# Kernel tuning notes

Hardware: AMD Instinct MI355X
Metric: run time of the kernel (lower is better)

Reference implementation:

```python
import jax, jax.numpy as jnp
import numpy as np

D = 2  # NUM_DIM (spatial dimension)


def _mlp(x, params, activate_final=False):
    n = len(params)
    for i, (w, b) in enumerate(params):
        x = x @ w + b
        if i < n - 1 or activate_final:
            x = jnp.tanh(x)
    return x


def _glorot(key, shape):
    fan_in, fan_out = shape[0], shape[-1]
    lim = np.sqrt(6.0 / (fan_in + fan_out)).astype(np.float32)
    return jax.random.uniform(key, shape, jnp.float32, -lim, lim)


def setup_inputs() -> dict:
    key = jax.random.key(0)
    ks = iter(jax.random.split(key, 40))
    B, N, M, K, P, C = 4, 32, 64, 16, 128, 2
    AW, TW, W = 64, 256, 128
    inp = {}
    inp['phase_coords'] = jax.random.normal(next(ks), (B, N, 2 * D), jnp.float32)
    inp['boundary_coords'] = jax.random.normal(next(ks), (B, M, 2 * D), jnp.float32)
    inp['boundary'] = jax.random.uniform(next(ks), (B, M), jnp.float32)
    inp['boundary_weights'] = jax.random.uniform(next(ks), (B, M), jnp.float32)
    inp['position_coords'] = jax.random.normal(next(ks), (B, P, D), jnp.float32)
    inp['sigma'] = jax.random.uniform(next(ks), (B, P, C), jnp.float32)
    inp['velocity_coords'] = jax.random.normal(next(ks), (B, K, D), jnp.float32)
    inp['velocity_weights'] = jax.random.uniform(next(ks), (B, K), jnp.float32)
    inp['scattering_kernel'] = jax.random.uniform(next(ks), (B, N, K), jnp.float32)
    inp['self_scattering_kernel'] = jax.random.uniform(next(ks), (B, K, K), jnp.float32)
    # attention MLP: input 2*D + 2 (coords ++ local frame) -> [64, 64, 1]
    inp['aw0'] = _glorot(next(ks), (2 * D + 2, AW)); inp['ab0'] = jnp.zeros((AW,), jnp.float32)
    inp['aw1'] = _glorot(next(ks), (AW, AW)); inp['ab1'] = jnp.zeros((AW,), jnp.float32)
    inp['aw2'] = _glorot(next(ks), (AW, 1)); inp['ab2'] = jnp.zeros((1,), jnp.float32)
    # transport MLP: input 4*D + C -> [256, 256, 128], activate_final=True
    inp['tw0'] = _glorot(next(ks), (4 * D + C, TW)); inp['tb0'] = jnp.zeros((TW,), jnp.float32)
    inp['tw1'] = _glorot(next(ks), (TW, TW)); inp['tb1'] = jnp.zeros((TW,), jnp.float32)
    inp['tw2'] = _glorot(next(ks), (TW, W)); inp['tb2'] = jnp.zeros((W,), jnp.float32)
    # scattering modules: res_block_depth=2 -> one stacked layer + one final layer
    inp['sw0'] = _glorot(next(ks), (W, W))
    inp['sb0'] = jax.random.uniform(next(ks), (W,), jnp.float32, -0.1, 0.1)
    inp['sw1'] = _glorot(next(ks), (W, W))
    inp['sb1'] = jax.random.uniform(next(ks), (W,), jnp.float32, -0.1, 0.1)
    inp['out_w'] = jax.random.uniform(next(ks), (W,), jnp.float32, -0.1, 0.1)
    return inp


def _forward(phase_coords, boundary_coords, boundary, boundary_weights,
             position_coords, sigma, velocity_coords, velocity_weights,
             scattering_kernel, self_scattering_kernel,
             aw0, ab0, aw1, ab1, aw2, ab2,
             tw0, tb0, tw1, tb1, tw2, tb2,
             sw0, sb0, sw1, sb1, out_w):
    B, N, _ = phase_coords.shape
    M = boundary_coords.shape[1]
    K = velocity_coords.shape[1]
    P = position_coords.shape[1]
    C = sigma.shape[-1]
    K1 = K + 1  # phase velocity v plus the Nv quadrature velocities

    x, v = phase_coords[..., :D], phase_coords[..., D:]          # (B,N,D)
    xp, vp = boundary_coords[..., :D], boundary_coords[..., D:]  # (B,M,D)

    # all velocities at which the transport MLP is evaluated: (B,N,K1,D)
    vall = jnp.concatenate(
        [v[:, :, None, :],
         jnp.broadcast_to(velocity_coords[:, None, :, :], (B, N, K, D))], axis=2)

    # ---- CoefficientNet (geometry-masked MLP attention over coeff positions) ----
    coords = jnp.concatenate(
        [jnp.broadcast_to(x[:, :, None, :], (B, N, K1, D)), vall], axis=-1)  # (B,N,K1,2D)
    ang_g = vall / jnp.sqrt(jnp.sum(vall ** 2, axis=-1, keepdims=True) + 1e-16)
    rel = x[:, :, None, :] - position_coords[:, None, :, :]                 # (B,N,P,D)
    rel_dist = jnp.sqrt(jnp.sum(rel ** 2, axis=-1) + 1e-16)                 # (B,N,P)
    pos_local = jnp.einsum('bnpd,bnkd->bnkp', rel, ang_g)                   # (B,N,K1,P)
    ang_local = pos_local / (rel_dist[:, :, None, :] + 1e-8)
    frames = jnp.stack([ang_local, pos_local], axis=-1)                     # (B,N,K1,P,2)
    qk = jnp.concatenate(
        [jnp.broadcast_to(coords[:, :, :, None, :], (B, N, K1, P, 2 * D)), frames], axis=-1)
    logits = _mlp(qk, [(aw0, ab0), (aw1, ab1), (aw2, ab2)])[..., 0]         # (B,N,K1,P)
    attn_w = jax.nn.softmax(jnp.where(pos_local > 0, logits, -1e30), axis=-1)
    coeff = jnp.exp(-jnp.einsum('bnkp,bpc->bnkc', attn_w, sigma))           # (B,N,K1,C)

    # ---- TransportModule: MLP + exp over (B,N,M,K1) ----
    t_in = jnp.concatenate([
        jnp.broadcast_to(x[:, :, None, None, :], (B, N, M, K1, D)),
        jnp.broadcast_to(vall[:, :, None, :, :], (B, N, M, K1, D)),
        jnp.broadcast_to(xp[:, None, :, None, :], (B, N, M, K1, D)),
        jnp.broadcast_to(vp[:, None, :, None, :], (B, N, M, K1, D)),
        jnp.broadcast_to(coeff[:, :, None, :, :], (B, N, M, K1, C)),
    ], axis=-1)
    g = jnp.exp(_mlp(t_in, [(tw0, tb0), (tw1, tb1), (tw2, tb2)], activate_final=True))
    act_v = g[:, :, :, 0, :]       # (B,N,M,W)  at the phase velocity
    act_vstar = g[:, :, :, 1:, :]  # (B,N,M,K,W) at the quadrature velocities

    rw_v = (1.0 - scattering_kernel) * velocity_weights[:, None, :]        # (B,N,K)
    rw_vs = (1.0 - self_scattering_kernel) * velocity_weights[:, None, :]  # (B,K,K)

    def scat_v(act, sw, sb):
        res = jnp.einsum('bnk,bnmkw->bnmw', rw_v, act)
        return jnp.tanh(jnp.einsum('iw,bnmw->bnmi', sw, res) + sb)

    def scat_vs(act, sw, sb):
        res = jnp.einsum('bij,bnmjw->bnmiw', rw_vs, act)
        return jnp.tanh(jnp.einsum('iw,bnmkw->bnmki', sw, res) + sb)

    # layer_stack block (res_block_depth - 1 = 1 layer, shared params within the layer)
    new_v = act_v + scat_v(act_vstar, sw0, sb0)
    act_vstar = act_vstar + scat_vs(act_vstar, sw0, sb0)
    act_v = new_v
    # final scattering module (fresh params) updating act_v with res_weights_v
    green = act_v + scat_v(act_vstar, sw1, sb1)

    gdot = jnp.einsum('bnmw,w->bnm', green, out_w)
    # quadrature over boundary points
    return jnp.einsum('bnm,bm->bn', gdot, boundary * boundary_weights)


def reference(phase_coords, boundary_coords, boundary, boundary_weights,
              position_coords, sigma, velocity_coords, velocity_weights,
              scattering_kernel, self_scattering_kernel,
              aw0, ab0, aw1, ab1, aw2, ab2,
              tw0, tb0, tw1, tb1, tw2, tb2,
              sw0, sb0, sw1, sb1, out_w):
    return _forward(phase_coords, boundary_coords, boundary, boundary_weights,
                    position_coords, sigma, velocity_coords, velocity_weights,
                    scattering_kernel, self_scattering_kernel,
                    aw0, ab0, aw1, ab1, aw2, ab2,
                    tw0, tb0, tw1, tb1, tw2, tb2,
                    sw0, sb0, sw1, sb1, out_w)
```

## Files before the change

### kernel.cpp

```cpp
#include <hip/hip_runtime.h>
#include <hip/hip_bf16.h>

#define BB 4
#define NN 32
#define MM 64
#define KK 16
#define KK1 17
#define PP 128
#define CC 2

typedef unsigned short ushort_t;
typedef unsigned int uint32;
typedef __attribute__((ext_vector_type(8))) short bhalf8;
typedef __attribute__((ext_vector_type(4))) float floatx4;

__device__ __forceinline__ float fast_tanh(float x) {
    float e = __expf(2.0f * x);
    return 1.0f - 2.0f / (e + 1.0f);
}
__device__ __forceinline__ ushort_t f2b(float f) {
    uint32 u = __float_as_uint(f);
    return (ushort_t)((u + 0x8000u) >> 16);
}
__device__ __forceinline__ float b2f(ushort_t h) {
    return __uint_as_float(((uint32)h) << 16);
}

__global__ void prep_kernel(const float* __restrict__ tw0, const float* __restrict__ tw1,
                            const float* __restrict__ tw2, const float* __restrict__ sw0,
                            const float* __restrict__ sw1, const float* __restrict__ aw0,
                            const float* __restrict__ aw1, const float* __restrict__ tb0,
                            const float* __restrict__ bcoord,
                            ushort_t* __restrict__ W1t, ushort_t* __restrict__ W2t,
                            ushort_t* __restrict__ S0t, ushort_t* __restrict__ S1t,
                            ushort_t* __restrict__ W0a, ushort_t* __restrict__ W1a,
                            ushort_t* __restrict__ w_ws) {
    int i = blockIdx.x * 256 + threadIdx.x;
    if (i < 65536) {
        int nn = i >> 8, k = i & 255;
        W1t[i] = f2b(tw1[k * 256 + nn]);
    } else if (i < 98304) {
        int j = i - 65536; int nn = j >> 8, k = j & 255;
        W2t[j] = f2b(tw2[k * 128 + nn]);
    } else if (i < 114688) {
        S0t[i - 98304] = f2b(sw0[i - 98304]);
    } else if (i < 131072) {
        S1t[i - 114688] = f2b(sw1[i - 114688]);
    } else if (i < 133120) {
        int j = i - 131072; int nn = j >> 5, k = j & 31;
        W0a[j] = (k < 6) ? f2b(aw0[k * 64 + nn]) : (ushort_t)0;
    } else if (i < 137216) {
        int j = i - 133120; int nn = j >> 6, k = j & 63;
        W1a[j] = f2b(aw1[k * 64 + nn]);
    } else if (i < 202752) {
        int j = i - 137216;
        int m = j >> 8, c = j & 255;
        float v = bcoord[m * 4 + 0] * tw0[4 * 256 + c]
                + bcoord[m * 4 + 1] * tw0[5 * 256 + c]
                + bcoord[m * 4 + 2] * tw0[6 * 256 + c]
                + bcoord[m * 4 + 3] * tw0[7 * 256 + c]
                + tb0[c];
        w_ws[j] = f2b(v);
    }
}

#define AH0S 72

__global__ __launch_bounds__(128, 4) void attn_kernel(
    const float* __restrict__ phase, const float* __restrict__ posc,
    const float* __restrict__ sigma, const float* __restrict__ velc,
    const ushort_t* __restrict__ W0a, const ushort_t* __restrict__ W1a,
    const float* __restrict__ ab0, const float* __restrict__ ab1,
    const float* __restrict__ aw2, const float* __restrict__ ab2,
    const float* __restrict__ tw0, ushort_t* __restrict__ u_ws)
{
    __shared__ __align__(16) ushort_t sAH[128 * AH0S];
    __shared__ float sPL[128];
    __shared__ float sLG[128];
    __shared__ float s_red[8];

    const int tid = threadIdx.x;
    const int wave = tid >> 6;
    const int lane = tid & 63;
    const int lrow = lane & 15;
    const int lkg  = lane >> 4;

    const int blk = blockIdx.x;
    const int b = blk / (NN * KK1);
    const int rem = blk % (NN * KK1);
    const int n = rem / KK1;
    const int k = rem % KK1;

    float x0, x1, va0, va1;
    {
        const int p = tid;
        x0 = phase[(b * NN + n) * 4 + 0];
        x1 = phase[(b * NN + n) * 4 + 1];
        if (k == 0) { va0 = phase[(b * NN + n) * 4 + 2]; va1 = phase[(b * NN + n) * 4 + 3]; }
        else { va0 = velc[(b * KK + (k - 1)) * 2 + 0]; va1 = velc[(b * KK + (k - 1)) * 2 + 1]; }
        const float inv = rsqrtf(va0 * va0 + va1 * va1 + 1e-16f);
        const float ag0 = va0 * inv, ag1 = va1 * inv;
        const float px = posc[(b * PP + p) * 2 + 0];
        const float py = posc[(b * PP + p) * 2 + 1];
        const float r0 = x0 - px, r1 = x1 - py;
        const float rd = sqrtf(r0 * r0 + r1 * r1 + 1e-16f);
        const float pl = r0 * ag0 + r1 * ag1;
        const float al = pl / (rd + 1e-8f);
        sPL[p] = pl;
        bhalf8 f0;
        f0[0] = (short)f2b(x0); f0[1] = (short)f2b(x1);
        f0[2] = (short)f2b(va0); f0[3] = (short)f2b(va1);
        f0[4] = (short)f2b(al); f0[5] = (short)f2b(pl);
        f0[6] = 0; f0[7] = 0;
        bhalf8 z = {0, 0, 0, 0, 0, 0, 0, 0};
        *(bhalf8*)&sAH[p * 32 + 0] = f0;
        *(bhalf8*)&sAH[p * 32 + 8] = z;
        *(bhalf8*)&sAH[p * 32 + 16] = z;
        *(bhalf8*)&sAH[p * 32 + 24] = z;
    }
    __syncthreads();

    {
        float b0v[4];
        #pragma unroll
        for (int j = 0; j < 4; ++j) b0v[j] = ab0[j * 16 + lrow];
        bhalf8 a[4];
        #pragma unroll
        for (int mtl = 0; mtl < 4; ++mtl)
            a[mtl] = *(const bhalf8*)&sAH[(wave * 64 + mtl * 16 + lrow) * 32 + lkg * 8];
        __syncthreads();
        #pragma unroll
        for (int j = 0; j < 4; ++j) {
            bhalf8 bf = *(const bhalf8*)(W0a + (j * 16 + lrow) * 32 + lkg * 8);
            #pragma unroll
            for (int mtl = 0; mtl < 4; ++mtl) {
                floatx4 c = {0.f, 0.f, 0.f, 0.f};
                c = __builtin_amdgcn_mfma_f32_16x16x32_bf16(a[mtl], bf, c, 0, 0, 0);
                #pragma unroll
                for (int q = 0; q < 4; ++q) {
                    int row = wave * 64 + mtl * 16 + lkg * 4 + q;
                    sAH[row * AH0S + j * 16 + lrow] = f2b(fast_tanh(c[q] + b0v[j]));
                }
            }
        }
    }
    __syncthreads();

    {
        float b1v[4], w2v[4];
        #pragma unroll
        for (int j = 0; j < 4; ++j) { b1v[j] = ab1[j * 16 + lrow]; w2v[j] = aw2[j * 16 + lrow]; }
        bhalf8 a0[4], a1[4];
        #pragma unroll
        for (int mtl = 0; mtl < 4; ++mtl) {
            int base = (wave * 64 + mtl * 16 + lrow) * AH0S;
            a0[mtl] = *(const bhalf8*)&sAH[base + lkg * 8];
            a1[mtl] = *(const bhalf8*)&sAH[base + 32 + lkg * 8];
        }
        float s[4][4];
        #pragma unroll
        for (int mtl = 0; mtl < 4; ++mtl)
            #pragma unroll
            for (int q = 0; q < 4; ++q) s[mtl][q] = 0.0f;
        #pragma unroll
        for (int j = 0; j < 4; ++j) {
            bhalf8 bf0 = *(const bhalf8*)(W1a + (j * 16 + lrow) * 64 + lkg * 8);
            bhalf8 bf1 = *(const bhalf8*)(W1a + (j * 16 + lrow) * 64 + 32 + lkg * 8);
            #pragma unroll
            for (int mtl = 0; mtl < 4; ++mtl) {
                floatx4 c = {0.f, 0.f, 0.f, 0.f};
                c = __builtin_amdgcn_mfma_f32_16x16x32_bf16(a0[mtl], bf0, c, 0, 0, 0);
                c = __builtin_amdgcn_mfma_f32_16x16x32_bf16(a1[mtl], bf1, c, 0, 0, 0);
                #pragma unroll
                for (int q = 0; q < 4; ++q)
                    s[mtl][q] += fast_tanh(c[q] + b1v[j]) * w2v[j];
            }
        }
        #pragma unroll
        for (int mask = 1; mask <= 8; mask <<= 1)
            #pragma unroll
            for (int mtl = 0; mtl < 4; ++mtl)
                #pragma unroll
                for (int q = 0; q < 4; ++q)
                    s[mtl][q] += __shfl_xor(s[mtl][q], mask, 64);
        if (lrow == 0) {
            #pragma unroll
            for (int mtl = 0; mtl < 4; ++mtl)
                #pragma unroll
                for (int q = 0; q < 4; ++q)
                    sLG[wave * 64 + mtl * 16 + lkg * 4 + q] = s[mtl][q];
        }
    }
    __syncthreads();

    {
        const int p = tid;
        const float ml = (sPL[p] > 0.0f) ? (sLG[p] + ab2[0]) : -1e30f;
        const int wid = wave;
        float mv = ml;
        for (int o = 32; o > 0; o >>= 1) mv = fmaxf(mv, __shfl_xor(mv, o, 64));
        if (lane == 0) s_red[wid] = mv;
        __syncthreads();
        mv = fmaxf(s_red[0], s_red[1]);

        const float ew = __expf(ml - mv);
        float sv = ew;
        for (int o = 32; o > 0; o >>= 1) sv += __shfl_xor(sv, o, 64);
        if (lane == 0) s_red[2 + wid] = sv;
        __syncthreads();
        sv = s_red[2] + s_red[3];
        const float attn = ew / sv;

        float s0 = attn * sigma[(b * PP + p) * 2 + 0];
        float s1 = attn * sigma[(b * PP + p) * 2 + 1];
        for (int o = 32; o > 0; o >>= 1) { s0 += __shfl_xor(s0, o, 64); s1 += __shfl_xor(s1, o, 64); }
        if (lane == 0) { s_red[4 + wid] = s0; s_red[6 + wid] = s1; }
        __syncthreads();

        const float cc0 = __expf(-(s_red[4] + s_red[5]));
        const float cc1 = __expf(-(s_red[6] + s_red[7]));
        const int ubase = ((b * NN + n) * KK1 + k) * 256;
        for (int cc = tid; cc < 256; cc += 128) {
            float uv = x0 * tw0[cc] + x1 * tw0[256 + cc]
                     + va0 * tw0[512 + cc] + va1 * tw0[768 + cc]
                     + cc0 * tw0[2048 + cc] + cc1 * tw0[2304 + cc];
            u_ws[ubase + cc] = f2b(uv);
        }
    }
}

#define H0S  264
#define H1S  136
#define GTSs 40
#define AS2S 136
#define V2S  40

#define U_H0A  0
#define U_H1A  8976
#define U_AS   13600
#define U_GTS  0
#define U_GV   5120
#define U_NEWV 5376
#define U_AS2  5632
#define U_V2T  10256
#define U_A2S  15376
#define U_A3   0
#define F_BBW  7944
#define F_RED  7946

__global__ __launch_bounds__(256, 4) void transport_kernel(
    const float* __restrict__ boundary, const float* __restrict__ bweights,
    const float* __restrict__ vweights, const float* __restrict__ scat,
    const float* __restrict__ selfscat,
    const ushort_t* __restrict__ W1t, const ushort_t* __restrict__ W2t,
    const ushort_t* __restrict__ S0t, const ushort_t* __restrict__ S1t,
    const float* __restrict__ tb1, const float* __restrict__ tb2,
    const float* __restrict__ sb0, const float* __restrict__ sb1,
    const float* __restrict__ outw,
    const ushort_t* __restrict__ u_ws, const ushort_t* __restrict__ w_ws,
    float* __restrict__ out)
{
    __shared__ __align__(16) ushort_t smem[15900];
    float* smf = (float*)smem;

    const int tid = threadIdx.x;
    const int wave = tid >> 6;
    const int lane = tid & 63;
    const int lrow = lane & 15;
    const int lkg  = lane >> 4;

    const int blk = blockIdx.x;
    const int b  = blk >> 10;
    const int n  = (blk >> 5) & 31;
    const int mg = blk & 31;
    const int m0 = mg * 2;
    const int bn = b * NN + n;

    if (tid < 2)
        smf[F_BBW + tid] = boundary[b * MM + m0 + tid] * bweights[b * MM + m0 + tid];

    for (int idx = tid; idx < 17 * 32; idx += 256) {
        int i = idx >> 5, c = idx & 31;
        float val = 0.0f;
        if (c < 16) {
            float vw = vweights[b * KK + c];
            val = (i < 16) ? (1.0f - selfscat[(b * KK + i) * KK + c]) * vw
                           : (1.0f - scat[bn * KK + c]) * vw;
        }
        smem[U_AS + idx] = f2b(val);
    }

    for (int idx = tid; idx < 34 * 32; idx += 256) {
        int row = idx >> 5, oct = idx & 31;
        int ml = (row >= 17);
        int k = row - ml * 17;
        bhalf8 uu = *(const bhalf8*)(u_ws + (bn * KK1 + k) * 256 + oct * 8);
        bhalf8 ww = *(const bhalf8*)(w_ws + (b * MM + m0 + ml) * 256 + oct * 8);
        bhalf8 hh;
        #pragma unroll
        for (int jj = 0; jj < 8; ++jj)
            hh[jj] = (short)f2b(fast_tanh(b2f((ushort_t)uu[jj]) + b2f((ushort_t)ww[jj])));
        *(bhalf8*)&smem[U_H0A + row * H0S + oct * 8] = hh;
    }
    __syncthreads();

    floatx4 c2[2][3];
    #pragma unroll
    for (int j = 0; j < 2; ++j)
        #pragma unroll
        for (int mt = 0; mt < 3; ++mt) c2[j][mt] = (floatx4){0.f, 0.f, 0.f, 0.f};

    for (int chunk = 0; chunk < 2; ++chunk) {
        if (chunk) __syncthreads();
        floatx4 c1[2][3];
        #pragma unroll
        for (int j = 0; j < 2; ++j)
            #pragma unroll
            for (int mt = 0; mt < 3; ++mt) c1[j][mt] = (floatx4){0.f, 0.f, 0.f, 0.f};
        #pragma unroll
        for (int ks = 0; ks < 8; ++ks) {
            bhalf8 a[3];
            #pragma unroll
            for (int mt = 0; mt < 3; ++mt)
                a[mt] = *(const bhalf8*)&smem[U_H0A + (mt * 16 + lrow) * H0S + ks * 32 + lkg * 8];
            #pragma unroll
            for (int j = 0; j < 2; ++j) {
                int colt = chunk * 8 + wave * 2 + j;
                bhalf8 bf = *(const bhalf8*)(W1t + (colt * 16 + lrow) * 256 + ks * 32 + lkg * 8);
                #pragma unroll
                for (int mt = 0; mt < 3; ++mt)
                    c1[j][mt] = __builtin_amdgcn_mfma_f32_16x16x32_bf16(a[mt], bf, c1[j][mt], 0, 0, 0);
            }
        }
        #pragma unroll
        for (int j = 0; j < 2; ++j) {
            const int lcol = (wave * 2 + j) * 16 + lrow;
            const float bb = tb1[chunk * 128 + lcol];
            #pragma unroll
            for (int mt = 0; mt < 3; ++mt)
                #pragma unroll
                for (int q = 0; q < 4; ++q) {
                    int row = mt * 16 + lkg * 4 + q;
                    if (row < 34)
                        smem[U_H1A + row * H1S + lcol] = f2b(fast_tanh(c1[j][mt][q] + bb));
                }
        }
        __syncthreads();
        #pragma unroll
        for (int ks2 = 0; ks2 < 4; ++ks2) {
            bhalf8 a[3];
            #pragma unroll
            for (int mt = 0; mt < 3; ++mt)
                a[mt] = *(const bhalf8*)&smem[U_H1A + (mt * 16 + lrow) * H1S + ks2 * 32 + lkg * 8];
            #pragma unroll
            for (int j = 0; j < 2; ++j) {
                bhalf8 bf = *(const bhalf8*)(W2t + ((wave * 2 + j) * 16 + lrow) * 256
                                             + chunk * 128 + ks2 * 32 + lkg * 8);
                #pragma unroll
                for (int mt = 0; mt < 3; ++mt)
                    c2[j][mt] = __builtin_amdgcn_mfma_f32_16x16x32_bf16(a[mt], bf, c2[j][mt], 0, 0, 0);
            }
        }
    }

    for (int idx = tid; idx < 1024; idx += 256)
        smem[U_GTS + (idx >> 3) * GTSs + 32 + (idx & 7)] = 0;
    {
        #pragma unroll
        for (int j = 0; j < 2; ++j) {
            const int col = (wave * 2 + j) * 16 + lrow;
            const float bb = tb2[col];
            #pragma unroll
            for (int mt = 0; mt < 3; ++mt)
                #pragma unroll
                for (int q = 0; q < 4; ++q) {
                    int row = mt * 16 + lkg * 4 + q;
                    if (row < 34) {
                        int ml = (row >= 17);
                        int k = row - ml * 17;
                        float g = __expf(fast_tanh(c2[j][mt][q] + bb));
                        if (k == 0) smem[U_GV + ml * 128 + col] = f2b(g);
                        else        smem[U_GTS + col * GTSs + ml * 16 + (k - 1)] = f2b(g);
                    }
                }
        }
    }
    __syncthreads();

    for (int idx = tid; idx < 512; idx += 256) {
        int r = idx >> 5, c = idx & 31;
        smem[U_A2S + idx] = ((c >> 4) == r) ? smem[U_AS + 16 * 32 + (c & 15)] : (ushort_t)0;
    }
    {
        bhalf8 a0 = *(const bhalf8*)&smem[U_AS + lrow * 32 + lkg * 8];
        bhalf8 a1 = *(const bhalf8*)&smem[U_AS + (16 + lrow) * 32 + lkg * 8];
        for (int m = 0; m < 2; ++m) {
            #pragma unroll
            for (int j = 0; j < 2; ++j) {
                int nt = 2 * wave + j;
                bhalf8 bf = *(const bhalf8*)&smem[U_GTS + (nt * 16 + lrow) * GTSs + m * 16 + lkg * 8];
                #pragma unroll
                for (int mt = 0; mt < 2; ++mt) {
                    floatx4 c = {0.f, 0.f, 0.f, 0.f};
                    c = __builtin_amdgcn_mfma_f32_16x16x32_bf16(mt ? a1 : a0, bf, c, 0, 0, 0);
                    #pragma unroll
                    for (int q = 0; q < 4; ++q) {
                        int ic = mt * 16 + lkg * 4 + q;
                        if (ic < 17) {
                            int r2 = (ic == 16) ? m * 17 : m * 17 + 1 + ic;
                            smem[U_AS2 + r2 * AS2S + nt * 16 + lrow] = f2b(c[q]);
                        }
                    }
                }
            }
        }
    }
    __syncthreads();

    {
        floatx4 c3[2][3];
        #pragma unroll
        for (int j = 0; j < 2; ++j)
            #pragma unroll
            for (int mt = 0; mt < 3; ++mt) c3[j][mt] = (floatx4){0.f, 0.f, 0.f, 0.f};
        #pragma unroll
        for (int ks = 0; ks < 4; ++ks) {
            bhalf8 a[3];
            #pragma unroll
            for (int mt = 0; mt < 3; ++mt)
                a[mt] = *(const bhalf8*)&smem[U_AS2 + (mt * 16 + lrow) * AS2S + ks * 32 + lkg * 8];
            #pragma unroll
            for (int j = 0; j < 2; ++j) {
                bhalf8 bf = *(const bhalf8*)(S0t + ((2 * wave + j) * 16 + lrow) * 128 + ks * 32 + lkg * 8);
                #pragma unroll
                for (int mt = 0; mt < 3; ++mt)
                    c3[j][mt] = __builtin_amdgcn_mfma_f32_16x16x32_bf16(a[mt], bf, c3[j][mt], 0, 0, 0);
            }
        }
        #pragma unroll
        for (int j = 0; j < 2; ++j) {
            const int col = (2 * wave + j) * 16 + lrow;
            const float bb = sb0[col];
            #pragma unroll
            for (int mt = 0; mt < 3; ++mt)
                #pragma unroll
                for (int q = 0; q < 4; ++q) {
                    int r2 = mt * 16 + lkg * 4 + q;
                    if (r2 < 34) {
                        int m = (r2 >= 17);
                        int i2 = r2 - m * 17;
                        float val = fast_tanh(c3[j][mt][q] + bb);
                        if (i2 == 0) {
                            smem[U_NEWV + m * 128 + col] =
                                f2b(b2f(smem[U_GV + m * 128 + col]) + val);
                        } else {
                            int j2 = i2 - 1;
                            smem[U_V2T + col * V2S + m * 16 + j2] =
                                f2b(b2f(smem[U_GTS + col * GTSs + m * 16 + j2]) + val);
                        }
                    }
                }
        }
    }
    __syncthreads();

    {
        bhalf8 a = *(const bhalf8*)&smem[U_A2S + lrow * 32 + lkg * 8];
        #pragma unroll
        for (int j = 0; j < 2; ++j) {
            int nt = 2 * wave + j;
            bhalf8 bf = *(const bhalf8*)&smem[U_V2T + (nt * 16 + lrow) * V2S + lkg * 8];
            floatx4 c = {0.f, 0.f, 0.f, 0.f};
            c = __builtin_amdgcn_mfma_f32_16x16x32_bf16(a, bf, c, 0, 0, 0);
            #pragma unroll
            for (int q = 0; q < 4; ++q) {
                int r = lkg * 4 + q;
                smem[U_A3 + r * AS2S + nt * 16 + lrow] = f2b(c[q]);
            }
        }
    }
    __syncthreads();

    float acc = 0.0f;
    {
        bhalf8 a[4];
        #pragma unroll
        for (int ks = 0; ks < 4; ++ks)
            a[ks] = *(const bhalf8*)&smem[U_A3 + lrow * AS2S + ks * 32 + lkg * 8];
        #pragma unroll
        for (int j = 0; j < 2; ++j) {
            int nt = 2 * wave + j;
            float s1v = sb1[nt * 16 + lrow];
            float owv = outw[nt * 16 + lrow];
            floatx4 c = {0.f, 0.f, 0.f, 0.f};
            #pragma unroll
            for (int ks = 0; ks < 4; ++ks) {
                bhalf8 bf = *(const bhalf8*)(S1t + (nt * 16 + lrow) * 128 + ks * 32 + lkg * 8);
                c = __builtin_amdgcn_mfma_f32_16x16x32_bf16(a[ks], bf, c, 0, 0, 0);
            }
            #pragma unroll
            for (int q = 0; q < 4; ++q) {
                int r = lkg * 4 + q;
                if (r < 2) {
                    int col = nt * 16 + lrow;
                    float green = b2f(smem[U_NEWV + r * 128 + col]) + fast_tanh(c[q] + s1v);
                    acc += green * owv * smf[F_BBW + r];
                }
            }
        }
    }
    for (int o = 32; o > 0; o >>= 1) acc += __shfl_xor(acc, o, 64);
    if (lane == 0) smf[F_RED + wave] = acc;
    __syncthreads();
    if (tid == 0) {
        float tot = smf[F_RED + 0] + smf[F_RED + 1] + smf[F_RED + 2] + smf[F_RED + 3];
        atomicAdd(&out[bn], tot);
    }
}

extern "C" void kernel_launch(void* const* d_in, const int* in_sizes, int n_in,
                              void* d_out, int out_size, void* d_ws, size_t ws_size,
                              hipStream_t stream) {
    const float* phase    = (const float*)d_in[0];
    const float* bcoord   = (const float*)d_in[1];
    const float* boundary = (const float*)d_in[2];
    const float* bweights = (const float*)d_in[3];
    const float* posc     = (const float*)d_in[4];
    const float* sigma    = (const float*)d_in[5];
    const float* velc     = (const float*)d_in[6];
    const float* vweights = (const float*)d_in[7];
    const float* scat     = (const float*)d_in[8];
    const float* selfscat = (const float*)d_in[9];
    const float* aw0 = (const float*)d_in[10];
    const float* ab0 = (const float*)d_in[11];
    const float* aw1 = (const float*)d_in[12];
    const float* ab1 = (const float*)d_in[13];
    const float* aw2 = (const float*)d_in[14];
    const float* ab2 = (const float*)d_in[15];
    const float* tw0 = (const float*)d_in[16];
    const float* tb0 = (const float*)d_in[17];
    const float* tw1 = (const float*)d_in[18];
    const float* tb1 = (const float*)d_in[19];
    const float* tw2 = (const float*)d_in[20];
    const float* tb2 = (const float*)d_in[21];
    const float* sw0 = (const float*)d_in[22];
    const float* sb0 = (const float*)d_in[23];
    const float* sw1 = (const float*)d_in[24];
    const float* sb1 = (const float*)d_in[25];
    const float* outw = (const float*)d_in[26];

    float* out = (float*)d_out;
    char* ws = (char*)d_ws;
    ushort_t* W1t  = (ushort_t*)(ws + 0);
    ushort_t* W2t  = (ushort_t*)(ws + 131072);
    ushort_t* S0t  = (ushort_t*)(ws + 196608);
    ushort_t* S1t  = (ushort_t*)(ws + 229376);
    ushort_t* W0a  = (ushort_t*)(ws + 262144);
    ushort_t* W1a  = (ushort_t*)(ws + 266240);
    ushort_t* u_ws = (ushort_t*)(ws + 274432);
    ushort_t* w_ws = (ushort_t*)(ws + 1388544);

    hipMemsetAsync(d_out, 0, (size_t)out_size * sizeof(float), stream);

    prep_kernel<<<792, 256, 0, stream>>>(tw0, tw1, tw2, sw0, sw1, aw0, aw1, tb0, bcoord,
                                         W1t, W2t, S0t, S1t, W0a, W1a, w_ws);

    attn_kernel<<<BB * NN * KK1, 128, 0, stream>>>(
        phase, posc, sigma, velc, W0a, W1a, ab0, ab1, aw2, ab2, tw0, u_ws);

    transport_kernel<<<BB * NN * 32, 256, 0, stream>>>(
        boundary, bweights, vweights, scat, selfscat,
        W1t, W2t, S0t, S1t, tb1, tb2, sb0, sb1, outw, u_ws, w_ws, out);
}
```

Measured before the change: 287.7 us.

## Fuse weight-prep and attention kernels into one launch with 256-thread blocks

Merges the weight-conversion prep kernel into the attention kernel as extra trailing blocks, removing one kernel launch and its serialization. The attention MLP weights are now converted to bf16 inline from fp32 global memory instead of being read from a prepped buffer. Attention blocks widen from 128 to 256 threads, with four waves each handling 32 rows, so the final u_ws write uses one column per thread. This costs redundant per-block weight conversion and leaves half the threads idle in the softmax phase.

New measurement: 287.9 us. No clear change (+0.1%).

```diff
diff --git a/kernel.cpp b/kernel.cpp
--- a/kernel.cpp
+++ b/kernel.cpp
@@ -26,66 +26,66 @@
     return __uint_as_float(((uint32)h) << 16);
 }
 
-__global__ void prep_kernel(const float* __restrict__ tw0, const float* __restrict__ tw1,
-                            const float* __restrict__ tw2, const float* __restrict__ sw0,
-                            const float* __restrict__ sw1, const float* __restrict__ aw0,
-                            const float* __restrict__ aw1, const float* __restrict__ tb0,
-                            const float* __restrict__ bcoord,
-                            ushort_t* __restrict__ W1t, ushort_t* __restrict__ W2t,
-                            ushort_t* __restrict__ S0t, ushort_t* __restrict__ S1t,
-                            ushort_t* __restrict__ W0a, ushort_t* __restrict__ W1a,
-                            ushort_t* __restrict__ w_ws) {
-    int i = blockIdx.x * 256 + threadIdx.x;
-    if (i < 65536) {
-        int nn = i >> 8, k = i & 255;
-        W1t[i] = f2b(tw1[k * 256 + nn]);
-    } else if (i < 98304) {
-        int j = i - 65536; int nn = j >> 8, k = j & 255;
-        W2t[j] = f2b(tw2[k * 128 + nn]);
-    } else if (i < 114688) {
-        S0t[i - 98304] = f2b(sw0[i - 98304]);
-    } else if (i < 131072) {
-        S1t[i - 114688] = f2b(sw1[i - 114688]);
-    } else if (i < 133120) {
-        int j = i - 131072; int nn = j >> 5, k = j & 31;
-        W0a[j] = (k < 6) ? f2b(aw0[k * 64 + nn]) : (ushort_t)0;
-    } else if (i < 137216) {
-        int j = i - 133120; int nn = j >> 6, k = j & 63;
-        W1a[j] = f2b(aw1[k * 64 + nn]);
-    } else if (i < 202752) {
-        int j = i - 137216;
-        int m = j >> 8, c = j & 255;
-        float v = bcoord[m * 4 + 0] * tw0[4 * 256 + c]
-                + bcoord[m * 4 + 1] * tw0[5 * 256 + c]
-                + bcoord[m * 4 + 2] * tw0[6 * 256 + c]
-                + bcoord[m * 4 + 3] * tw0[7 * 256 + c]
-                + tb0[c];
-        w_ws[j] = f2b(v);
-    }
-}
+#define NATTN (BB * NN * KK1)
+#define NPREP 768
 
 #define AH0S 72
 
-__global__ __launch_bounds__(128, 4) void attn_kernel(
+__global__ __launch_bounds__(256, 4) void prep_attn_kernel(
     const float* __restrict__ phase, const float* __restrict__ posc,
     const float* __restrict__ sigma, const float* __restrict__ velc,
-    const ushort_t* __restrict__ W0a, const ushort_t* __restrict__ W1a,
+    const float* __restrict__ aw0, const float* __restrict__ aw1,
     const float* __restrict__ ab0, const float* __restrict__ ab1,
     const float* __restrict__ aw2, const float* __restrict__ ab2,
-    const float* __restrict__ tw0, ushort_t* __restrict__ u_ws)
+    const float* __restrict__ tw0, ushort_t* __restrict__ u_ws,
+    const float* __restrict__ tw1, const float* __restrict__ tw2,
+    const float* __restrict__ sw0, const float* __restrict__ sw1,
+    const float* __restrict__ tb0, const float* __restrict__ bcoord,
+    ushort_t* __restrict__ W1t, ushort_t* __restrict__ W2t,
+    ushort_t* __restrict__ S0t, ushort_t* __restrict__ S1t,
+    ushort_t* __restrict__ w_ws)
 {
     __shared__ __align__(16) ushort_t sAH[128 * AH0S];
     __shared__ float sPL[128];
     __shared__ float sLG[128];
-    __shared__ float s_red[8];
-
+    __shared__ float s_red[16];
+
+    const int blk = blockIdx.x;
     const int tid = threadIdx.x;
+
+    if (blk >= NATTN) {
+        int i = (blk - NATTN) * 256 + tid;
+        if (i < 65536) {
+            int nn = i >> 8, k = i & 255;
+            W1t[i] = f2b(tw1[k * 256 + nn]);
+        } else if (i < 98304) {
+            int j = i - 65536; int nn = j >> 7, k = j & 127;
+            (void)nn; (void)k;
+            int jj = i - 65536;
+            int col = jj >> 8, kk = jj & 255;
+            W2t[jj] = f2b(tw2[kk * 128 + col]);
+        } else if (i < 114688) {
+            S0t[i - 98304] = f2b(sw0[i - 98304]);
+        } else if (i < 131072) {
+            S1t[i - 114688] = f2b(sw1[i - 114688]);
+        } else if (i < 196608) {
+            int j = i - 131072;
+            int m = j >> 8, c = j & 255;
+            float v = bcoord[m * 4 + 0] * tw0[4 * 256 + c]
+                    + bcoord[m * 4 + 1] * tw0[5 * 256 + c]
+                    + bcoord[m * 4 + 2] * tw0[6 * 256 + c]
+                    + bcoord[m * 4 + 3] * tw0[7 * 256 + c]
+                    + tb0[c];
+            w_ws[j] = f2b(v);
+        }
+        return;
+    }
+
     const int wave = tid >> 6;
     const int lane = tid & 63;
     const int lrow = lane & 15;
     const int lkg  = lane >> 4;
 
-    const int blk = blockIdx.x;
     const int b = blk / (NN * KK1);
     const int rem = blk % (NN * KK1);
     const int n = rem / KK1;
@@ -93,7 +93,7 @@
 
     float x0, x1, va0, va1;
     {
-        const int p = tid;
+        const int p = tid & 127;
         x0 = phase[(b * NN + n) * 4 + 0];
         x1 = phase[(b * NN + n) * 4 + 1];
         if (k == 0) { va0 = phase[(b * NN + n) * 4 + 2]; va1 = phase[(b * NN + n) * 4 + 3]; }
@@ -106,17 +106,19 @@
         const float rd = sqrtf(r0 * r0 + r1 * r1 + 1e-16f);
         const float pl = r0 * ag0 + r1 * ag1;
         const float al = pl / (rd + 1e-8f);
-        sPL[p] = pl;
-        bhalf8 f0;
-        f0[0] = (short)f2b(x0); f0[1] = (short)f2b(x1);
-        f0[2] = (short)f2b(va0); f0[3] = (short)f2b(va1);
-        f0[4] = (short)f2b(al); f0[5] = (short)f2b(pl);
-        f0[6] = 0; f0[7] = 0;
-        bhalf8 z = {0, 0, 0, 0, 0, 0, 0, 0};
-        *(bhalf8*)&sAH[p * 32 + 0] = f0;
-        *(bhalf8*)&sAH[p * 32 + 8] = z;
-        *(bhalf8*)&sAH[p * 32 + 16] = z;
-        *(bhalf8*)&sAH[p * 32 + 24] = z;
+        if (tid < 128) {
+            sPL[p] = pl;
+            bhalf8 f0;
+            f0[0] = (short)f2b(x0); f0[1] = (short)f2b(x1);
+            f0[2] = (short)f2b(va0); f0[3] = (short)f2b(va1);
+            f0[4] = (short)f2b(al); f0[5] = (short)f2b(pl);
+            f0[6] = 0; f0[7] = 0;
+            bhalf8 z = {0, 0, 0, 0, 0, 0, 0, 0};
+            *(bhalf8*)&sAH[p * 32 + 0] = f0;
+            *(bhalf8*)&sAH[p * 32 + 8] = z;
+            *(bhalf8*)&sAH[p * 32 + 16] = z;
+            *(bhalf8*)&sAH[p * 32 + 24] = z;
+        }
     }
     __syncthreads();
 
@@ -124,21 +126,27 @@
         float b0v[4];
         #pragma unroll
         for (int j = 0; j < 4; ++j) b0v[j] = ab0[j * 16 + lrow];
-        bhalf8 a[4];
-        #pragma unroll
-        for (int mtl = 0; mtl < 4; ++mtl)
-            a[mtl] = *(const bhalf8*)&sAH[(wave * 64 + mtl * 16 + lrow) * 32 + lkg * 8];
+        bhalf8 a[2];
+        #pragma unroll
+        for (int mtl = 0; mtl < 2; ++mtl)
+            a[mtl] = *(const bhalf8*)&sAH[(wave * 32 + mtl * 16 + lrow) * 32 + lkg * 8];
         __syncthreads();
         #pragma unroll
         for (int j = 0; j < 4; ++j) {
-            bhalf8 bf = *(const bhalf8*)(W0a + (j * 16 + lrow) * 32 + lkg * 8);
-            #pragma unroll
-            for (int mtl = 0; mtl < 4; ++mtl) {
+            bhalf8 bf;
+            #pragma unroll
+            for (int i2 = 0; i2 < 8; ++i2) {
+                int kk2 = lkg * 8 + i2;
+                float v = (kk2 < 6) ? aw0[kk2 * 64 + j * 16 + lrow] : 0.0f;
+                bf[i2] = (short)f2b(v);
+            }
+            #pragma unroll
+            for (int mtl = 0; mtl < 2; ++mtl) {
                 floatx4 c = {0.f, 0.f, 0.f, 0.f};
                 c = __builtin_amdgcn_mfma_f32_16x16x32_bf16(a[mtl], bf, c, 0, 0, 0);
                 #pragma unroll
                 for (int q = 0; q < 4; ++q) {
-                    int row = wave * 64 + mtl * 16 + lkg * 4 + q;
+                    int row = wave * 32 + mtl * 16 + lkg * 4 + q;
                     sAH[row * AH0S + j * 16 + lrow] = f2b(fast_tanh(c[q] + b0v[j]));
                 }
             }
@@ -150,24 +158,29 @@
         float b1v[4], w2v[4];
         #pragma unroll
         for (int j = 0; j < 4; ++j) { b1v[j] = ab1[j * 16 + lrow]; w2v[j] = aw2[j * 16 + lrow]; }
-        bhalf8 a0[4], a1[4];
-        #pragma unroll
-        for (int mtl = 0; mtl < 4; ++mtl) {
-            int base = (wave * 64 + mtl * 16 + lrow) * AH0S;
+        bhalf8 a0[2], a1[2];
+        #pragma unroll
+        for (int mtl = 0; mtl < 2; ++mtl) {
+            int base = (wave * 32 + mtl * 16 + lrow) * AH0S;
             a0[mtl] = *(const bhalf8*)&sAH[base + lkg * 8];
             a1[mtl] = *(const bhalf8*)&sAH[base + 32 + lkg * 8];
         }
-        float s[4][4];
-        #pragma unroll
-        for (int mtl = 0; mtl < 4; ++mtl)
+        float s[2][4];
+        #pragma unroll
+        for (int mtl = 0; mtl < 2; ++mtl)
             #pragma unroll
             for (int q = 0; q < 4; ++q) s[mtl][q] = 0.0f;
         #pragma unroll
         for (int j = 0; j < 4; ++j) {
-            bhalf8 bf0 = *(const bhalf8*)(W1a + (j * 16 + lrow) * 64 + lkg * 8);
-            bhalf8 bf1 = *(const bhalf8*)(W1a + (j * 16 + lrow) * 64 + 32 + lkg * 8);
-            #pragma unroll
-            for (int mtl = 0; mtl < 4; ++mtl) {
+            const int col = j * 16 + lrow;
+            bhalf8 bf0, bf1;
+            #pragma unroll
+            for (int i2 = 0; i2 < 8; ++i2) {
+                bf0[i2] = (short)f2b(aw1[(lkg * 8 + i2) * 64 + col]);
+                bf1[i2] = (short)f2b(aw1[(32 + lkg * 8 + i2) * 64 + col]);
+            }
+            #pragma unroll
+            for (int mtl = 0; mtl < 2; ++mtl) {
                 floatx4 c = {0.f, 0.f, 0.f, 0.f};
                 c = __builtin_amdgcn_mfma_f32_16x16x32_bf16(a0[mtl], bf0, c, 0, 0, 0);
                 c = __builtin_amdgcn_mfma_f32_16x16x32_bf16(a1[mtl], bf1, c, 0, 0, 0);
@@ -179,53 +192,51 @@
         #pragma unroll
         for (int mask = 1; mask <= 8; mask <<= 1)
             #pragma unroll
-            for (int mtl = 0; mtl < 4; ++mtl)
+            for (int mtl = 0; mtl < 2; ++mtl)
                 #pragma unroll
                 for (int q = 0; q < 4; ++q)
                     s[mtl][q] += __shfl_xor(s[mtl][q], mask, 64);
         if (lrow == 0) {
             #pragma unroll
-            for (int mtl = 0; mtl < 4; ++mtl)
+            for (int mtl = 0; mtl < 2; ++mtl)
                 #pragma unroll
                 for (int q = 0; q < 4; ++q)
-                    sLG[wave * 64 + mtl * 16 + lkg * 4 + q] = s[mtl][q];
-        }
-    }
-    __syncthreads();
-
-    {
-        const int p = tid;
-        const float ml = (sPL[p] > 0.0f) ? (sLG[p] + ab2[0]) : -1e30f;
-        const int wid = wave;
+                    sLG[wave * 32 + mtl * 16 + lkg * 4 + q] = s[mtl][q];
+        }
+    }
+    __syncthreads();
+
+    {
+        const int p = tid & 127;
+        const float ml = (tid < 128 && sPL[p] > 0.0f) ? (sLG[p] + ab2[0]) : -1e30f;
         float mv = ml;
         for (int o = 32; o > 0; o >>= 1) mv = fmaxf(mv, __shfl_xor(mv, o, 64));
-        if (lane == 0) s_red[wid] = mv;
+        if (lane == 0) s_red[wave] = mv;
         __syncthreads();
-        mv = fmaxf(s_red[0], s_red[1]);
-
-        const float ew = __expf(ml - mv);
+        mv = fmaxf(fmaxf(s_red[0], s_red[1]), fmaxf(s_red[2], s_red[3]));
+
+        const float ew = (tid < 128) ? __expf(ml - mv) : 0.0f;
         float sv = ew;
         for (int o = 32; o > 0; o >>= 1) sv += __shfl_xor(sv, o, 64);
-        if (lane == 0) s_red[2 + wid] = sv;
+        if (lane == 0) s_red[4 + wave] = sv;
         __syncthreads();
-        sv = s_red[2] + s_red[3];
+        sv = s_red[4] + s_red[5] + s_red[6] + s_red[7];
         const float attn = ew / sv;
 
-        float s0 = attn * sigma[(b * PP + p) * 2 + 0];
-        float s1 = attn * sigma[(b * PP + p) * 2 + 1];
+        float s0 = (tid < 128) ? attn * sigma[(b * PP + p) * 2 + 0] : 0.0f;
+        float s1 = (tid < 128) ? attn * sigma[(b * PP + p) * 2 + 1] : 0.0f;
         for (int o = 32; o > 0; o >>= 1) { s0 += __shfl_xor(s0, o, 64); s1 += __shfl_xor(s1, o, 64); }
-        if (lane == 0) { s_red[4 + wid] = s0; s_red[6 + wid] = s1; }
+        if (lane == 0) { s_red[8 + wave] = s0; s_red[12 + wave] = s1; }
         __syncthreads();
 
-        const float cc0 = __expf(-(s_red[4] + s_red[5]));
-        const float cc1 = __expf(-(s_red[6] + s_red[7]));
+        const float cc0 = __expf(-(s_red[8] + s_red[9] + s_red[10] + s_red[11]));
+        const float cc1 = __expf(-(s_red[12] + s_red[13] + s_red[14] + s_red[15]));
         const int ubase = ((b * NN + n) * KK1 + k) * 256;
-        for (int cc = tid; cc < 256; cc += 128) {
-            float uv = x0 * tw0[cc] + x1 * tw0[256 + cc]
-                     + va0 * tw0[512 + cc] + va1 * tw0[768 + cc]
-                     + cc0 * tw0[2048 + cc] + cc1 * tw0[2304 + cc];
-            u_ws[ubase + cc] = f2b(uv);
-        }
+        const int cc = tid;
+        float uv = x0 * tw0[cc] + x1 * tw0[256 + cc]
+                 + va0 * tw0[512 + cc] + va1 * tw0[768 + cc]
+                 + cc0 * tw0[2048 + cc] + cc1 * tw0[2304 + cc];
+        u_ws[ubase + cc] = f2b(uv);
     }
 }
 
@@ -555,18 +566,14 @@
     ushort_t* W2t  = (ushort_t*)(ws + 131072);
     ushort_t* S0t  = (ushort_t*)(ws + 196608);
     ushort_t* S1t  = (ushort_t*)(ws + 229376);
-    ushort_t* W0a  = (ushort_t*)(ws + 262144);
-    ushort_t* W1a  = (ushort_t*)(ws + 266240);
-    ushort_t* u_ws = (ushort_t*)(ws + 274432);
-    ushort_t* w_ws = (ushort_t*)(ws + 1388544);
+    ushort_t* u_ws = (ushort_t*)(ws + 262144);
+    ushort_t* w_ws = (ushort_t*)(ws + 1376256);
 
     hipMemsetAsync(d_out, 0, (size_t)out_size * sizeof(float), stream);
 
-    prep_kernel<<<792, 256, 0, stream>>>(tw0, tw1, tw2, sw0, sw1, aw0, aw1, tb0, bcoord,
-                                         W1t, W2t, S0t, S1t, W0a, W1a, w_ws);
-
-    attn_kernel<<<BB * NN * KK1, 128, 0, stream>>>(
-        phase, posc, sigma, velc, W0a, W1a, ab0, ab1, aw2, ab2, tw0, u_ws);
+    prep_attn_kernel<<<NATTN + NPREP, 256, 0, stream>>>(
+        phase, posc, sigma, velc, aw0, aw1, ab0, ab1, aw2, ab2, tw0, u_ws,
+        tw1, tw2, sw0, sw1, tb0, bcoord, W1t, W2t, S0t, S1t, w_ws);
 
     transport_kernel<<<BB * NN * 32, 256, 0, stream>>>(
         boundary, bweights, vweights, scat, selfscat,
```
